# Optimization experiments

Measured on AMD Instinct MI355X. Metric: run time of the kernel, lower is better.

Reference implementation:

```python
import jax, jax.numpy as jnp
import numpy as np

D_MODEL = 1024
NUM_HEADS = 16

def setup_inputs() -> dict:
    key = jax.random.key(0)
    ks = jax.random.split(key, 9)
    d = D_MODEL
    s = 0.02
    return {
        "x": jax.random.normal(ks[0], (2, 2048, d), dtype=jnp.float32),
        "wq": jax.random.normal(ks[1], (d, d), dtype=jnp.float32) * s,
        "bq": jax.random.normal(ks[2], (d,), dtype=jnp.float32) * s,
        "wk": jax.random.normal(ks[3], (d, d), dtype=jnp.float32) * s,
        "bk": jax.random.normal(ks[4], (d,), dtype=jnp.float32) * s,
        "wv": jax.random.normal(ks[5], (d, d), dtype=jnp.float32) * s,
        "bv": jax.random.normal(ks[6], (d,), dtype=jnp.float32) * s,
        "wo": jax.random.normal(ks[7], (d, d), dtype=jnp.float32) * s,
        "bo": jax.random.normal(ks[8], (d,), dtype=jnp.float32) * s,
    }

def reference(x, wq, bq, wk, bk, wv, bv, wo, bo) -> jnp.ndarray:
    b, s, d = x.shape
    h = NUM_HEADS
    dk = d // h
    # projections (torch Linear: x @ W^T + b)
    q = x @ wq.T + bq
    k = x @ wk.T + bk
    v = x @ wv.T + bv
    # split heads -> [b, h, s, dk]
    q = q.reshape(b, s, h, dk).transpose(0, 2, 1, 3)
    k = k.reshape(b, s, h, dk).transpose(0, 2, 1, 3)
    v = v.reshape(b, s, h, dk).transpose(0, 2, 1, 3)
    scale = jnp.sqrt(jnp.asarray(dk, dtype=x.dtype))
    scores = jnp.einsum('bhqd,bhkd->bhqk', q, k) / scale
    causal = jnp.tril(jnp.ones((s, s), dtype=bool))  # [s, s]
    scores = jnp.where(causal[None, None], scores, jnp.asarray(-jnp.inf, dtype=x.dtype))
    attn = jax.nn.softmax(scores, axis=-1)
    out = jnp.einsum('bhqk,bhkd->bhqd', attn, v)
    out = out.transpose(0, 2, 1, 3).reshape(b, s, d)
    return out @ wo.T + bo
```

## Files before the change

### kernel.cpp

```cpp
#include <hip/hip_runtime.h>

#define D_MODEL 1024
#define NHEAD   16
#define DK      64
#define BATCH   2
#define SEQ     2048
#define M_TOT   (BATCH*SEQ)

typedef unsigned short u16;
typedef unsigned int   u32;
typedef __attribute__((ext_vector_type(8))) __bf16 bf16x8;
typedef __attribute__((ext_vector_type(8))) u16   u16x8;
typedef __attribute__((ext_vector_type(4))) u16   u16x4;
typedef __attribute__((ext_vector_type(4))) float f32x4;

typedef const __attribute__((address_space(1))) u32* gas_ptr;
typedef __attribute__((address_space(3))) u32*       las_ptr;

__device__ __forceinline__ void gload16(const u16* g, u16* l) {
  __builtin_amdgcn_global_load_lds((gas_ptr)g, (las_ptr)l, 16, 0, 0);
}

__device__ __forceinline__ u16 bfc(float f) {
  union { __bf16 h; u16 u; } v; v.h = (__bf16)f; return v.u;
}

#define BAR() do { \
  __builtin_amdgcn_sched_barrier(0); \
  __builtin_amdgcn_s_barrier(); \
  __builtin_amdgcn_sched_barrier(0); \
} while (0)

__global__ void cvt_all(const float* __restrict__ x,
                        const float* __restrict__ wq, const float* __restrict__ wk,
                        const float* __restrict__ wv, const float* __restrict__ wo,
                        u16* __restrict__ xbf, u16* __restrict__ wbf) {
  const int y = blockIdx.y;
  const float* src;
  u16* dst;
  int n8;
  if (y == 0)      { src = x;  dst = xbf;                n8 = M_TOT * D_MODEL / 8; }
  else if (y == 1) { src = wq; dst = wbf;                n8 = 1024 * 1024 / 8; }
  else if (y == 2) { src = wk; dst = wbf + 1 * 1048576;  n8 = 1024 * 1024 / 8; }
  else if (y == 3) { src = wv; dst = wbf + 2 * 1048576;  n8 = 1024 * 1024 / 8; }
  else             { src = wo; dst = wbf + 3 * 1048576;  n8 = 1024 * 1024 / 8; }
  for (int i = blockIdx.x * blockDim.x + threadIdx.x; i < n8; i += gridDim.x * blockDim.x) {
    const float4* s = (const float4*)src + (size_t)i * 2;
    float4 a = s[0], b = s[1];
    u16x8 o;
    o[0]=bfc(a.x); o[1]=bfc(a.y); o[2]=bfc(a.z); o[3]=bfc(a.w);
    o[4]=bfc(b.x); o[5]=bfc(b.y); o[6]=bfc(b.z); o[7]=bfc(b.w);
    *((u16x8*)dst + i) = o;
  }
}

#define QSCALE 0.18033688011112042f

__global__ __launch_bounds__(256) void qkv_gemm(
    const u16* __restrict__ xbf, const u16* __restrict__ wbf,
    const float* __restrict__ bq, const float* __restrict__ bk, const float* __restrict__ bv,
    u16* __restrict__ qws, u16* __restrict__ kws, u16* __restrict__ vtws)
{
  __shared__ u16 la[2 * 128 * 32];
  __shared__ u16 lb[2 * 64 * 32];
  const int flat = blockIdx.x;
  const int xcd  = flat & 7;
  const int loc  = flat >> 3;
  const int z    = loc >> 6;
  const int rem  = loc & 63;
  const int nbase = (rem & 15) * 64;
  const int mbase = (xcd * 4 + (rem >> 4)) * 128;
  const u16*  A    = xbf;
  const u16*  Bm   = wbf + (size_t)z * 1024 * 1024;
  const float* bias = (z == 0) ? bq : (z == 1) ? bk : bv;

  const int tid  = threadIdx.x;
  const int lane = tid & 63;
  const int wid  = tid >> 6;
  const int wr   = (wid >> 1) * 64, wc = (wid & 1) * 32;
  const int lr   = lane & 15, lg = lane >> 4;
  const int srow = tid >> 2;
  const int sc   = tid & 3;
  const int sdst = srow * 32 + sc * 8;
  const int ssrc = (sc ^ ((srow >> 1) & 3)) * 8;
  const int csw  = (lg ^ ((lr >> 1) & 3)) * 8;

  f32x4 acc[4][2];
  #pragma unroll
  for (int i = 0; i < 4; ++i) { acc[i][0] = (f32x4){0,0,0,0}; acc[i][1] = (f32x4){0,0,0,0}; }

  {
    gload16(&A [(size_t)(mbase + srow)      * 1024 + ssrc], &la[sdst]);
    gload16(&A [(size_t)(mbase + srow + 64) * 1024 + ssrc], &la[64*32 + sdst]);
    gload16(&Bm[(size_t)(nbase + srow)      * 1024 + ssrc], &lb[sdst]);
  }
  __syncthreads();
  int cur = 0;
  for (int k0 = 0; k0 < 1024; k0 += 32) {
    if (k0 + 32 < 1024) {
      const int nb = cur ^ 1;
      gload16(&A [(size_t)(mbase + srow)      * 1024 + k0 + 32 + ssrc], &la[nb*4096 + sdst]);
      gload16(&A [(size_t)(mbase + srow + 64) * 1024 + k0 + 32 + ssrc], &la[nb*4096 + 64*32 + sdst]);
      gload16(&Bm[(size_t)(nbase + srow)      * 1024 + k0 + 32 + ssrc], &lb[nb*2048 + sdst]);
    }
    bf16x8 af[4], bfr[2];
    #pragma unroll
    for (int i = 0; i < 4; ++i)
      af[i] = *(const bf16x8*)&la[cur*4096 + (wr + i*16 + lr)*32 + csw];
    #pragma unroll
    for (int j = 0; j < 2; ++j)
      bfr[j] = *(const bf16x8*)&lb[cur*2048 + (wc + j*16 + lr)*32 + csw];
    #pragma unroll
    for (int i = 0; i < 4; ++i)
      #pragma unroll
      for (int j = 0; j < 2; ++j)
        acc[i][j] = __builtin_amdgcn_mfma_f32_16x16x32_bf16(af[i], bfr[j], acc[i][j], 0, 0, 0);
    __syncthreads();
    cur ^= 1;
  }

  #pragma unroll
  for (int i = 0; i < 4; ++i) {
    #pragma unroll
    for (int j = 0; j < 2; ++j) {
      int gn = nbase + wc + j*16 + lr;
      float bs = bias[gn];
      int h = gn >> 6, d = gn & 63;
      int gm0 = mbase + wr + i*16 + lg*4;
      int bb = gm0 >> 11, s0 = gm0 & 2047;
      if (z == 2) {
        u16x4 vk;
        #pragma unroll
        for (int r = 0; r < 4; ++r) vk[r] = bfc(acc[i][j][r] + bs);
        *(u16x4*)&vtws[(((size_t)(bb*NHEAD + h)) * DK + d) * SEQ + s0] = vk;
      } else {
        #pragma unroll
        for (int r = 0; r < 4; ++r) {
          float v = acc[i][j][r] + bs;
          if (z == 0) qws[(((size_t)(bb*NHEAD + h)) * SEQ + s0 + r) * DK + d] = bfc(v * QSCALE);
          else        kws[(((size_t)(bb*NHEAD + h)) * SEQ + s0 + r) * DK + d] = bfc(v);
        }
      }
    }
  }
}

__global__ __launch_bounds__(256) void out_gemm(
    const u16* __restrict__ ows, const u16* __restrict__ wobf,
    const float* __restrict__ bo, float* __restrict__ out)
{
  __shared__ u16 la[2 * 64 * 64];
  __shared__ u16 lb[2 * 64 * 64];
  const int flat = blockIdx.x;
  const int xcd  = flat & 7;
  const int loc  = flat >> 3;
  const int nbase = (loc & 15) * 64;
  const int mbase = (xcd * 8 + (loc >> 4)) * 64;
  const int tid  = threadIdx.x;
  const int lane = tid & 63;
  const int wid  = tid >> 6;
  const int wr   = (wid >> 1) * 32, wc = (wid & 1) * 32;
  const int lr   = lane & 15, lg = lane >> 4;
  const int srow = tid >> 3;
  const int sc   = tid & 7;
  const int sdst = srow * 64 + sc * 8;
  const int ssrc = (sc ^ (srow & 7)) * 8;
  const int lsw  = lr & 7;

  f32x4 acc[2][2];
  acc[0][0] = (f32x4){0,0,0,0}; acc[0][1] = (f32x4){0,0,0,0};
  acc[1][0] = (f32x4){0,0,0,0}; acc[1][1] = (f32x4){0,0,0,0};

  {
    gload16(&ows [(size_t)(mbase + srow)      * 1024 + ssrc], &la[sdst]);
    gload16(&ows [(size_t)(mbase + srow + 32) * 1024 + ssrc], &la[32*64 + sdst]);
    gload16(&wobf[(size_t)(nbase + srow)      * 1024 + ssrc], &lb[sdst]);
    gload16(&wobf[(size_t)(nbase + srow + 32) * 1024 + ssrc], &lb[32*64 + sdst]);
  }
  __syncthreads();
  int cur = 0;
  for (int k0 = 0; k0 < 1024; k0 += 64) {
    if (k0 + 64 < 1024) {
      const int nb = cur ^ 1;
      gload16(&ows [(size_t)(mbase + srow)      * 1024 + k0 + 64 + ssrc], &la[nb*4096 + sdst]);
      gload16(&ows [(size_t)(mbase + srow + 32) * 1024 + k0 + 64 + ssrc], &la[nb*4096 + 32*64 + sdst]);
      gload16(&wobf[(size_t)(nbase + srow)      * 1024 + k0 + 64 + ssrc], &lb[nb*4096 + sdst]);
      gload16(&wobf[(size_t)(nbase + srow + 32) * 1024 + k0 + 64 + ssrc], &lb[nb*4096 + 32*64 + sdst]);
    }
    bf16x8 af[2][2], bfr[2][2];
    #pragma unroll
    for (int kk = 0; kk < 2; ++kk) {
      #pragma unroll
      for (int i = 0; i < 2; ++i)
        af[i][kk] = *(const bf16x8*)&la[cur*4096 + (wr + i*16 + lr)*64 + (((kk*4 + lg) ^ lsw) * 8)];
      #pragma unroll
      for (int j = 0; j < 2; ++j)
        bfr[j][kk] = *(const bf16x8*)&lb[cur*4096 + (wc + j*16 + lr)*64 + (((kk*4 + lg) ^ lsw) * 8)];
    }
    #pragma unroll
    for (int kk = 0; kk < 2; ++kk)
      #pragma unroll
      for (int i = 0; i < 2; ++i)
        #pragma unroll
        for (int j = 0; j < 2; ++j)
          acc[i][j] = __builtin_amdgcn_mfma_f32_16x16x32_bf16(af[i][kk], bfr[j][kk], acc[i][j], 0, 0, 0);
    __syncthreads();
    cur ^= 1;
  }

  #pragma unroll
  for (int i = 0; i < 2; ++i) {
    #pragma unroll
    for (int j = 0; j < 2; ++j) {
      int gn = nbase + wc + j*16 + lr;
      float bs = bo[gn];
      #pragma unroll
      for (int r = 0; r < 4; ++r) {
        int gm = mbase + wr + i*16 + lg*4 + r;
        out[(size_t)gm * 1024 + gn] = acc[i][j][r] + bs;
      }
    }
  }
}

__global__ __launch_bounds__(256) void attn_kernel(
    const u16* __restrict__ qws, const u16* __restrict__ kws,
    const u16* __restrict__ vtws, u16* __restrict__ ows)
{
  __shared__ u16 kbuf[2 * 64 * 64];
  __shared__ u16 vbuf[2 * 64 * 64];
  __shared__ u16 pbuf[4 * 16 * 64];
  const int flat = blockIdx.x;
  const int r    = flat & 7;
  const int g    = flat >> 3;
  const int bh_l = g >> 5;
  const int qp   = g & 31;
  const int qt   = (bh_l & 1) ? qp : (31 - qp);
  const int bh   = r * 4 + bh_l;
  const int b = bh >> 4, h = bh & 15;
  const int tid = threadIdx.x, wid = tid >> 6, lane = tid & 63;
  const int lr = lane & 15, lg = lane >> 4;
  const u16* Q  = qws  + (size_t)(b * NHEAD + h) * SEQ * DK;
  const u16* K  = kws  + (size_t)(b * NHEAD + h) * SEQ * DK;
  const u16* Vt = vtws + (size_t)(b * NHEAD + h) * DK * SEQ;

  const int sr  = tid >> 3;
  const int sc8 = (tid & 7) * 8;
  const int c0s = ((tid & 7) ^ (sr & 7)) * 8;
  const int c1s = ((tid & 7) ^ ((sr + 32) & 7)) * 8;

  #define STAGE(u, bi) do { \
    const int kb_ = (u) * 64; \
    const int off_ = (bi) * 4096; \
    gload16(&K[(size_t)(kb_ + sr) * DK + c0s],        &kbuf[off_ + sr * 64 + sc8]); \
    gload16(&K[(size_t)(kb_ + sr + 32) * DK + c1s],   &kbuf[off_ + (sr + 32) * 64 + sc8]); \
    gload16(&Vt[(size_t)sr * SEQ + kb_ + c0s],        &vbuf[off_ + sr * 64 + sc8]); \
    gload16(&Vt[(size_t)(sr + 32) * SEQ + kb_ + c1s], &vbuf[off_ + (sr + 32) * 64 + sc8]); \
  } while (0)
  #define CH(m) ((((m)*4 + lg) ^ (lr & 7)) * 8)

  const int qbase  = qt * 64 + wid * 16;
  const int q_glob = qbase + lr;

  bf16x8 qf0 = *(const bf16x8*)&Q[(size_t)q_glob * DK + lg * 8];
  bf16x8 qf1 = *(const bf16x8*)&Q[(size_t)q_glob * DK + 32 + lg * 8];

  f32x4 oacc[4];
  #pragma unroll
  for (int t = 0; t < 4; ++t) oacc[t] = (f32x4){0.f, 0.f, 0.f, 0.f};
  float l_run = 0.f;

  STAGE(0, 0);
  if (qt >= 1) STAGE(1, 1);

  for (int t = 0; t <= qt; ++t) {
    if (t < qt) asm volatile("s_waitcnt vmcnt(4)" ::: "memory");
    else        asm volatile("s_waitcnt vmcnt(0)" ::: "memory");
    BAR();

    const int diag = (t == qt);
    const int nsub = diag ? (wid + 1) : 4;
    const int cb = (t & 1) * 4096;

    f32x4 sacc[4];
    __builtin_amdgcn_s_setprio(1);
    #pragma unroll
    for (int ts = 0; ts < 4; ++ts) {
      if (ts >= nsub) continue;
      bf16x8 kf0 = *(const bf16x8*)&kbuf[cb + (ts*16 + lr) * 64 + CH(0)];
      bf16x8 kf1 = *(const bf16x8*)&kbuf[cb + (ts*16 + lr) * 64 + CH(1)];
      f32x4 s0 = (f32x4){0.f, 0.f, 0.f, 0.f};
      s0 = __builtin_amdgcn_mfma_f32_16x16x32_bf16(kf0, qf0, s0, 0, 0, 0);
      s0 = __builtin_amdgcn_mfma_f32_16x16x32_bf16(kf1, qf1, s0, 0, 0, 0);
      sacc[ts] = s0;
    }
    __builtin_amdgcn_s_setprio(0);
    if (diag) {
      const int ts = wid;
      #pragma unroll
      for (int r2 = 0; r2 < 4; ++r2)
        if (lg * 4 + r2 > lr) sacc[ts][r2] = -1e30f;
    }
    #pragma unroll
    for (int ts = 0; ts < 4; ++ts) {
      if (ts >= nsub) continue;
      #pragma unroll
      for (int r2 = 0; r2 < 4; ++r2) {
        float p = __builtin_amdgcn_exp2f(sacc[ts][r2]);
        sacc[ts][r2] = p;
        l_run += p;
      }
    }

    #pragma unroll
    for (int ts = 0; ts < 4; ++ts) {
      u16x4 pk;
      if (ts < nsub) {
        pk[0] = bfc(sacc[ts][0]); pk[1] = bfc(sacc[ts][1]);
        pk[2] = bfc(sacc[ts][2]); pk[3] = bfc(sacc[ts][3]);
      } else {
        pk[0] = 0; pk[1] = 0; pk[2] = 0; pk[3] = 0;
      }
      const int pc = (((ts*2 + (lg >> 1)) ^ (lr & 7)) * 8) + (lg & 1) * 4;
      *(u16x4*)&pbuf[wid * 1024 + lr * 64 + pc] = pk;
    }
    asm volatile("s_waitcnt lgkmcnt(0)" ::: "memory");
    __builtin_amdgcn_sched_barrier(0);
    bf16x8 pf0 = *(const bf16x8*)&pbuf[wid * 1024 + lr * 64 + CH(0)];
    bf16x8 pf1 = *(const bf16x8*)&pbuf[wid * 1024 + lr * 64 + CH(1)];

    __builtin_amdgcn_s_setprio(1);
    #pragma unroll
    for (int td = 0; td < 4; ++td) {
      bf16x8 vf0 = *(const bf16x8*)&vbuf[cb + (td*16 + lr) * 64 + CH(0)];
      bf16x8 vf1 = *(const bf16x8*)&vbuf[cb + (td*16 + lr) * 64 + CH(1)];
      oacc[td] = __builtin_amdgcn_mfma_f32_16x16x32_bf16(vf0, pf0, oacc[td], 0, 0, 0);
      oacc[td] = __builtin_amdgcn_mfma_f32_16x16x32_bf16(vf1, pf1, oacc[td], 0, 0, 0);
    }
    __builtin_amdgcn_s_setprio(0);
    BAR();
    if (t + 2 <= qt) STAGE(t + 2, t & 1);
  }

  float l_tot = l_run;
  l_tot += __shfl_xor(l_tot, 16);
  l_tot += __shfl_xor(l_tot, 32);
  const float inv = 1.0f / l_tot;
  #pragma unroll
  for (int td = 0; td < 4; ++td) {
    u16x4 ok;
    #pragma unroll
    for (int r2 = 0; r2 < 4; ++r2) ok[r2] = bfc(oacc[td][r2] * inv);
    *(u16x4*)&ows[((size_t)(b * SEQ + q_glob)) * D_MODEL + h * DK + td*16 + lg*4] = ok;
  }
  #undef CH
  #undef STAGE
}

extern "C" void kernel_launch(void* const* d_in, const int* in_sizes, int n_in,
                              void* d_out, int out_size, void* d_ws, size_t ws_size,
                              hipStream_t stream) {
  const float* x  = (const float*)d_in[0];
  const float* wq = (const float*)d_in[1];
  const float* bq = (const float*)d_in[2];
  const float* wk = (const float*)d_in[3];
  const float* bk = (const float*)d_in[4];
  const float* wv = (const float*)d_in[5];
  const float* bv = (const float*)d_in[6];
  const float* wo = (const float*)d_in[7];
  const float* bo = (const float*)d_in[8];
  float* out = (float*)d_out;

  char* ws = (char*)d_ws;
  u16* qws  = (u16*)(ws + (size_t) 0 * (1 << 20));
  u16* kws  = (u16*)(ws + (size_t) 8 * (1 << 20));
  u16* vtws = (u16*)(ws + (size_t)16 * (1 << 20));
  u16* ows  = (u16*)(ws + (size_t)24 * (1 << 20));
  u16* xbf  = (u16*)(ws + (size_t)32 * (1 << 20));
  u16* wbf  = (u16*)(ws + (size_t)40 * (1 << 20));

  cvt_all<<<dim3(512, 5), 256, 0, stream>>>(x, wq, wk, wv, wo, xbf, wbf);

  qkv_gemm<<<dim3(1536, 1, 1), 256, 0, stream>>>(
      xbf, wbf, bq, bk, bv, qws, kws, vtws);

  attn_kernel<<<dim3(1024, 1, 1), 256, 0, stream>>>(qws, kws, vtws, ows);

  out_gemm<<<dim3(1024, 1, 1), 256, 0, stream>>>(
      ows, wbf + (size_t)3 * 1024 * 1024, bo, out);
}
```

Before: 108.6 us.

## Fuse fp32-to-bf16 conversion of x into QKV GEMM A-tile staging

Drops the separate conversion pass over x. The QKV GEMM now loads fp32 x rows into registers, converts them to bf16 and writes them to LDS after the MFMAs, while B still uses async global-to-LDS loads. This removes a 16MB read and 8MB write pass over x plus its bf16 round trip. The cost is that the GEMM reads twice the bytes for A, and since each x tile is read by 48 blocks (16 N-tiles times 3 projections), the fp32 x traffic grows. It also adds register pressure and conversion ALU work inside the main loop.

```diff
diff --git a/kernel.cpp b/kernel.cpp
--- a/kernel.cpp
+++ b/kernel.cpp
@@ -31,19 +31,13 @@
   __builtin_amdgcn_sched_barrier(0); \
 } while (0)
 
-__global__ void cvt_all(const float* __restrict__ x,
-                        const float* __restrict__ wq, const float* __restrict__ wk,
+__global__ void cvt_all(const float* __restrict__ wq, const float* __restrict__ wk,
                         const float* __restrict__ wv, const float* __restrict__ wo,
-                        u16* __restrict__ xbf, u16* __restrict__ wbf) {
+                        u16* __restrict__ wbf) {
   const int y = blockIdx.y;
-  const float* src;
-  u16* dst;
-  int n8;
-  if (y == 0)      { src = x;  dst = xbf;                n8 = M_TOT * D_MODEL / 8; }
-  else if (y == 1) { src = wq; dst = wbf;                n8 = 1024 * 1024 / 8; }
-  else if (y == 2) { src = wk; dst = wbf + 1 * 1048576;  n8 = 1024 * 1024 / 8; }
-  else if (y == 3) { src = wv; dst = wbf + 2 * 1048576;  n8 = 1024 * 1024 / 8; }
-  else             { src = wo; dst = wbf + 3 * 1048576;  n8 = 1024 * 1024 / 8; }
+  const float* src = (y == 0) ? wq : (y == 1) ? wk : (y == 2) ? wv : wo;
+  u16* dst = wbf + (size_t)y * 1048576;
+  const int n8 = 1024 * 1024 / 8;
   for (int i = blockIdx.x * blockDim.x + threadIdx.x; i < n8; i += gridDim.x * blockDim.x) {
     const float4* s = (const float4*)src + (size_t)i * 2;
     float4 a = s[0], b = s[1];
@@ -57,7 +51,7 @@
 #define QSCALE 0.18033688011112042f
 
 __global__ __launch_bounds__(256) void qkv_gemm(
-    const u16* __restrict__ xbf, const u16* __restrict__ wbf,
+    const float* __restrict__ x, const u16* __restrict__ wbf,
     const float* __restrict__ bq, const float* __restrict__ bk, const float* __restrict__ bv,
     u16* __restrict__ qws, u16* __restrict__ kws, u16* __restrict__ vtws)
 {
@@ -70,7 +64,6 @@
   const int rem  = loc & 63;
   const int nbase = (rem & 15) * 64;
   const int mbase = (xcd * 4 + (rem >> 4)) * 128;
-  const u16*  A    = xbf;
   const u16*  Bm   = wbf + (size_t)z * 1024 * 1024;
   const float* bias = (z == 0) ? bq : (z == 1) ? bk : bv;
 
@@ -85,23 +78,42 @@
   const int ssrc = (sc ^ ((srow >> 1) & 3)) * 8;
   const int csw  = (lg ^ ((lr >> 1) & 3)) * 8;
 
+  const float* xr0 = x + (size_t)(mbase + srow) * 1024;
+  const float* xr1 = x + (size_t)(mbase + srow + 64) * 1024;
+
   f32x4 acc[4][2];
   #pragma unroll
   for (int i = 0; i < 4; ++i) { acc[i][0] = (f32x4){0,0,0,0}; acc[i][1] = (f32x4){0,0,0,0}; }
 
-  {
-    gload16(&A [(size_t)(mbase + srow)      * 1024 + ssrc], &la[sdst]);
-    gload16(&A [(size_t)(mbase + srow + 64) * 1024 + ssrc], &la[64*32 + sdst]);
-    gload16(&Bm[(size_t)(nbase + srow)      * 1024 + ssrc], &lb[sdst]);
-  }
+  float4 ra0, ra1, ra2, ra3;
+  #define LOADA(k0_) do { \
+    ra0 = *(const float4*)&xr0[(k0_) + ssrc]; \
+    ra1 = *(const float4*)&xr0[(k0_) + ssrc + 4]; \
+    ra2 = *(const float4*)&xr1[(k0_) + ssrc]; \
+    ra3 = *(const float4*)&xr1[(k0_) + ssrc + 4]; \
+  } while (0)
+  #define WRITEA(bi) do { \
+    u16x8 w0, w1; \
+    w0[0]=bfc(ra0.x); w0[1]=bfc(ra0.y); w0[2]=bfc(ra0.z); w0[3]=bfc(ra0.w); \
+    w0[4]=bfc(ra1.x); w0[5]=bfc(ra1.y); w0[6]=bfc(ra1.z); w0[7]=bfc(ra1.w); \
+    w1[0]=bfc(ra2.x); w1[1]=bfc(ra2.y); w1[2]=bfc(ra2.z); w1[3]=bfc(ra2.w); \
+    w1[4]=bfc(ra3.x); w1[5]=bfc(ra3.y); w1[6]=bfc(ra3.z); w1[7]=bfc(ra3.w); \
+    *(u16x8*)&la[(bi)*4096 + sdst] = w0; \
+    *(u16x8*)&la[(bi)*4096 + 64*32 + sdst] = w1; \
+  } while (0)
+  #define STAGEB(k0_, bi) \
+    gload16(&Bm[(size_t)(nbase + srow) * 1024 + (k0_) + ssrc], &lb[(bi)*2048 + sdst])
+
+  LOADA(0);
+  STAGEB(0, 0);
+  WRITEA(0);
   __syncthreads();
+
   int cur = 0;
   for (int k0 = 0; k0 < 1024; k0 += 32) {
     if (k0 + 32 < 1024) {
-      const int nb = cur ^ 1;
-      gload16(&A [(size_t)(mbase + srow)      * 1024 + k0 + 32 + ssrc], &la[nb*4096 + sdst]);
-      gload16(&A [(size_t)(mbase + srow + 64) * 1024 + k0 + 32 + ssrc], &la[nb*4096 + 64*32 + sdst]);
-      gload16(&Bm[(size_t)(nbase + srow)      * 1024 + k0 + 32 + ssrc], &lb[nb*2048 + sdst]);
+      LOADA(k0 + 32);
+      STAGEB(k0 + 32, cur ^ 1);
     }
     bf16x8 af[4], bfr[2];
     #pragma unroll
@@ -115,9 +127,13 @@
       #pragma unroll
       for (int j = 0; j < 2; ++j)
         acc[i][j] = __builtin_amdgcn_mfma_f32_16x16x32_bf16(af[i], bfr[j], acc[i][j], 0, 0, 0);
+    if (k0 + 32 < 1024) WRITEA(cur ^ 1);
     __syncthreads();
     cur ^= 1;
   }
+  #undef LOADA
+  #undef WRITEA
+  #undef STAGEB
 
   #pragma unroll
   for (int i = 0; i < 4; ++i) {
@@ -376,13 +392,12 @@
   u16* kws  = (u16*)(ws + (size_t) 8 * (1 << 20));
   u16* vtws = (u16*)(ws + (size_t)16 * (1 << 20));
   u16* ows  = (u16*)(ws + (size_t)24 * (1 << 20));
-  u16* xbf  = (u16*)(ws + (size_t)32 * (1 << 20));
-  u16* wbf  = (u16*)(ws + (size_t)40 * (1 << 20));
-
-  cvt_all<<<dim3(512, 5), 256, 0, stream>>>(x, wq, wk, wv, wo, xbf, wbf);
+  u16* wbf  = (u16*)(ws + (size_t)32 * (1 << 20));
+
+  cvt_all<<<dim3(512, 4), 256, 0, stream>>>(wq, wk, wv, wo, wbf);
 
   qkv_gemm<<<dim3(1536, 1, 1), 256, 0, stream>>>(
-      xbf, wbf, bq, bk, bv, qws, kws, vtws);
+      x, wbf, bq, bk, bv, qws, kws, vtws);
 
   attn_kernel<<<dim3(1024, 1, 1), 256, 0, stream>>>(qws, kws, vtws, ows);
 
```

New measurement: 121.6 us. +12.0%, slower.

## Enlarge attention query tile to 128 rows with 8 waves per block

Applied to the files above, without the earlier changes.

The attention kernel now processes 128 query rows per block using 8 waves (512 threads) instead of 64 rows with 4 waves. Each K/V tile staged into shared memory is reused by twice as many waves, and each thread now issues one load per tensor per stage instead of two. The causal mask logic is generalized so each wave computes its own diagonal position per KV tile. This halves the grid to 512 blocks, which reduces occupancy granularity and may worsen load balance. Waves whose rows lie before a KV tile still wait at the barriers while doing nothing.

```diff
diff --git a/kernel.cpp b/kernel.cpp
--- a/kernel.cpp
+++ b/kernel.cpp
@@ -223,20 +223,21 @@
   }
 }
 
-__global__ __launch_bounds__(256) void attn_kernel(
+__global__ __launch_bounds__(512) void attn_kernel(
     const u16* __restrict__ qws, const u16* __restrict__ kws,
     const u16* __restrict__ vtws, u16* __restrict__ ows)
 {
   __shared__ u16 kbuf[2 * 64 * 64];
   __shared__ u16 vbuf[2 * 64 * 64];
-  __shared__ u16 pbuf[4 * 16 * 64];
+  __shared__ u16 pbuf[8 * 16 * 64];
   const int flat = blockIdx.x;
-  const int r    = flat & 7;
+  const int xcd  = flat & 7;
   const int g    = flat >> 3;
-  const int bh_l = g >> 5;
-  const int qp   = g & 31;
-  const int qt   = (bh_l & 1) ? qp : (31 - qp);
-  const int bh   = r * 4 + bh_l;
+  const int bh_l = g >> 4;
+  const int qp   = g & 15;
+  const int dir  = (bh_l >> 1) & 1;
+  const int qt   = dir ? qp : (15 - qp);
+  const int bh   = xcd * 4 + bh_l;
   const int b = bh >> 4, h = bh & 15;
   const int tid = threadIdx.x, wid = tid >> 6, lane = tid & 63;
   const int lr = lane & 15, lg = lane >> 4;
@@ -246,21 +247,17 @@
 
   const int sr  = tid >> 3;
   const int sc8 = (tid & 7) * 8;
-  const int c0s = ((tid & 7) ^ (sr & 7)) * 8;
-  const int c1s = ((tid & 7) ^ ((sr + 32) & 7)) * 8;
+  const int cs  = ((tid & 7) ^ (sr & 7)) * 8;
 
   #define STAGE(u, bi) do { \
     const int kb_ = (u) * 64; \
     const int off_ = (bi) * 4096; \
-    gload16(&K[(size_t)(kb_ + sr) * DK + c0s],        &kbuf[off_ + sr * 64 + sc8]); \
-    gload16(&K[(size_t)(kb_ + sr + 32) * DK + c1s],   &kbuf[off_ + (sr + 32) * 64 + sc8]); \
-    gload16(&Vt[(size_t)sr * SEQ + kb_ + c0s],        &vbuf[off_ + sr * 64 + sc8]); \
-    gload16(&Vt[(size_t)(sr + 32) * SEQ + kb_ + c1s], &vbuf[off_ + (sr + 32) * 64 + sc8]); \
+    gload16(&K[(size_t)(kb_ + sr) * DK + cs],  &kbuf[off_ + sr * 64 + sc8]); \
+    gload16(&Vt[(size_t)sr * SEQ + kb_ + cs],  &vbuf[off_ + sr * 64 + sc8]); \
   } while (0)
   #define CH(m) ((((m)*4 + lg) ^ (lr & 7)) * 8)
 
-  const int qbase  = qt * 64 + wid * 16;
-  const int q_glob = qbase + lr;
+  const int q_glob = qt * 128 + wid * 16 + lr;
 
   bf16x8 qf0 = *(const bf16x8*)&Q[(size_t)q_glob * DK + lg * 8];
   bf16x8 qf1 = *(const bf16x8*)&Q[(size_t)q_glob * DK + 32 + lg * 8];
@@ -270,16 +267,17 @@
   for (int t = 0; t < 4; ++t) oacc[t] = (f32x4){0.f, 0.f, 0.f, 0.f};
   float l_run = 0.f;
 
+  const int ntiles = 2 * qt + 2;
   STAGE(0, 0);
-  if (qt >= 1) STAGE(1, 1);
-
-  for (int t = 0; t <= qt; ++t) {
-    if (t < qt) asm volatile("s_waitcnt vmcnt(4)" ::: "memory");
-    else        asm volatile("s_waitcnt vmcnt(0)" ::: "memory");
+  STAGE(1, 1);
+
+  for (int t = 0; t < ntiles; ++t) {
+    if (t < ntiles - 1) asm volatile("s_waitcnt vmcnt(2)" ::: "memory");
+    else                asm volatile("s_waitcnt vmcnt(0)" ::: "memory");
     BAR();
 
-    const int diag = (t == qt);
-    const int nsub = diag ? (wid + 1) : 4;
+    const int rel  = qt * 8 + wid - t * 4;
+    const int nsub = rel >= 4 ? 4 : (rel < 0 ? 0 : rel + 1);
     const int cb = (t & 1) * 4096;
 
     f32x4 sacc[4];
@@ -295,11 +293,10 @@
       sacc[ts] = s0;
     }
     __builtin_amdgcn_s_setprio(0);
-    if (diag) {
-      const int ts = wid;
+    if (rel >= 0 && rel < 4) {
       #pragma unroll
       for (int r2 = 0; r2 < 4; ++r2)
-        if (lg * 4 + r2 > lr) sacc[ts][r2] = -1e30f;
+        if (lg * 4 + r2 > lr) sacc[rel][r2] = -1e30f;
     }
     #pragma unroll
     for (int ts = 0; ts < 4; ++ts) {
@@ -339,7 +336,7 @@
     }
     __builtin_amdgcn_s_setprio(0);
     BAR();
-    if (t + 2 <= qt) STAGE(t + 2, t & 1);
+    if (t + 2 < ntiles) STAGE(t + 2, t & 1);
   }
 
   float l_tot = l_run;
@@ -384,7 +381,7 @@
   qkv_gemm<<<dim3(1536, 1, 1), 256, 0, stream>>>(
       xbf, wbf, bq, bk, bv, qws, kws, vtws);
 
-  attn_kernel<<<dim3(1024, 1, 1), 256, 0, stream>>>(qws, kws, vtws, ows);
+  attn_kernel<<<dim3(512, 1, 1), 512, 0, stream>>>(qws, kws, vtws, ows);
 
   out_gemm<<<dim3(1024, 1, 1), 256, 0, stream>>>(
       ows, wbf + (size_t)3 * 1024 * 1024, bo, out);
```

After: 115.0 us. 1.06x slower.
